# Optimization experiments

Measured on AMD Instinct MI355X. Metric: run time of the kernel, lower is better.

Reference implementation:

```python
import jax, jax.numpy as jnp
import numpy as np

# dims
B, T, C = 8, 2048, 768          # batch, tokens, n_embed
E, K, H = 8, 2, 3072            # n_experts, top_k, n_mlp_hidden
LOAD = 1.25
CAP = int(LOAD * K * T // E)    # expert_capacity = 640
N_LAYER = 12


def setup_inputs() -> dict:
    key = jax.random.key(0)
    ks = jax.random.split(key, 6)
    s = 0.02
    s_proj = 0.02 * (2 * N_LAYER) ** (-0.5)
    return {
        "x": jax.random.normal(ks[0], (B, T, C), jnp.float32),
        "w_router": (jax.random.normal(ks[1], (C, E), jnp.float32) * s),
        "b_router": jnp.zeros((E,), jnp.float32),
        "w_c_fc": (jax.random.normal(ks[2], (E, C, H), jnp.float32) * s),
        "b_c_fc": jnp.zeros((E, 1, H), jnp.float32),
        "w_gate": (jax.random.normal(ks[3], (E, C, H), jnp.float32) * s),
        "b_gate": jnp.zeros((E, 1, H), jnp.float32),
        "w_c_proj": (jax.random.normal(ks[4], (E, H, C), jnp.float32) * s_proj),
        "b_c_proj": jnp.zeros((E, 1, C), jnp.float32),
    }


def _route(xb, probs):
    """Per-sequence top-k routing + capacity-based scatter dispatch.
    xb: [T, C], probs: [T, E] -> (topk_probs [T,K], pos [T,K], ei [T,K], buf [E,CAP,C])"""
    topk_probs, idx = jax.lax.top_k(probs, K)          # [T, K]
    ei = jnp.swapaxes(idx, 0, 1).ravel()               # [K*T], k-major like original
    oh = jax.nn.one_hot(ei, E, dtype=jnp.int32)        # [K*T, E]
    pos = jnp.cumsum(oh, axis=0) * oh - 1              # running slot per expert
    pos = jnp.max(jnp.swapaxes(pos.reshape(K, T, E), 0, 1), axis=2)  # [T, K]
    ei = jnp.swapaxes(ei.reshape(K, T), 0, 1)          # [T, K]
    xr = jnp.repeat(xb, K, axis=0)                     # [T*K, C], token-major
    # out-of-capacity positions (>= CAP) are dropped by jax scatter semantics,
    # matching the original module.
    buf = jnp.zeros((E, CAP, C), xb.dtype).at[ei.ravel(), pos.ravel()].set(xr)
    return topk_probs, pos, ei, buf


def reference(x, w_router, b_router, w_c_fc, b_c_fc, w_gate, b_gate,
              w_c_proj, b_c_proj):
    gate_logits = jnp.einsum("btc,ce->bte", x, w_router) + b_router
    gate_probs = jax.nn.softmax(gate_logits)
    topk_probs, pos, ei, buf = jax.vmap(_route)(x, gate_probs)  # buf: [B,E,CAP,C]

    # dispatch: expert-major layout (token permutation inside each expert is
    # irrelevant for the per-token expert MLP, so this is equivalent to the
    # original's sharding-oriented reshuffle)
    expert_inputs = jnp.swapaxes(buf, 0, 1).reshape(E, B * CAP, C)

    # grouped-GEMM SwiGLU experts
    h = jnp.einsum("eti,eih->eth", expert_inputs, w_c_fc) + b_c_fc
    g = jnp.einsum("eti,eih->eth", expert_inputs, w_gate) + b_gate
    o = jnp.einsum("eth,eho->eto", jax.nn.silu(h * g), w_c_proj) + b_c_proj

    eo = jnp.swapaxes(o.reshape(E, B, CAP, C), 0, 1)    # [B, E, CAP, C]

    def combine(eo_b, ei_b, pos_b, p_b):
        gathered = eo_b[ei_b, pos_b]                    # [T, K, C]
        return jnp.sum(p_b[..., None] * gathered, axis=1)

    return jax.vmap(combine)(eo, ei, pos, topk_probs)   # [B, T, C]
```

## Files before the change

### kernel.cpp

```cpp
#include <hip/hip_runtime.h>

typedef unsigned short u16;
typedef unsigned int u32;
using u16x4 = __attribute__((ext_vector_type(4))) u16;
using u16x8 = __attribute__((ext_vector_type(8))) u16;
using bf16x8 = __attribute__((ext_vector_type(8))) __bf16;
using f32x4 = __attribute__((ext_vector_type(4))) float;

#define B_ 8
#define T_ 2048
#define C_ 768
#define E_ 8
#define K_ 2
#define H_ 3072
#define CAP_ 640
#define M_ (B_ * CAP_)
#define HC_ 1024
#define NCHUNK_ (H_ / HC_)
#define OVF_MAX_ 32768

__device__ __forceinline__ u16 f2bf(float x) {
  u32 u = __float_as_uint(x);
  u32 r = (u + 0x7FFFu + ((u >> 16) & 1u)) >> 16;
  return (u16)r;
}
__device__ __forceinline__ float bf2f(u16 v) { return __uint_as_float(((u32)v) << 16); }

__device__ __forceinline__ void gl_lds16(const u16* g, u16* l) {
  __builtin_amdgcn_global_load_lds((const __attribute__((address_space(1))) u32*)g,
                                   (__attribute__((address_space(3))) u32*)l, 16, 0, 0);
}
__device__ __forceinline__ bf16x8 ldfrag(const u16* p) {
  return __builtin_bit_cast(bf16x8, *(const u16x8*)p);
}

__global__ void wconv_transpose(const float* __restrict__ in, u16* __restrict__ out,
                                int R, int Cc) {
  __shared__ float tile[32][33];
  const float* inE = in + (size_t)blockIdx.z * R * Cc;
  u16* outE = out + (size_t)blockIdx.z * R * Cc;
  int tx = threadIdx.x & 31, ty = threadIdx.x >> 5;
  int r0 = blockIdx.y * 32, c0 = blockIdx.x * 32;
#pragma unroll
  for (int j = 0; j < 4; j++)
    tile[ty + j * 8][tx] = inE[(size_t)(r0 + ty + j * 8) * Cc + (c0 + tx)];
  __syncthreads();
#pragma unroll
  for (int j = 0; j < 4; j++)
    outE[(size_t)(c0 + ty + j * 8) * R + (r0 + tx)] = f2bf(tile[tx][ty + j * 8]);
}

__global__ void router_kernel(const float* __restrict__ x, const float* __restrict__ wr,
                              const float* __restrict__ br, float* __restrict__ tkp,
                              int* __restrict__ tki) {
  int bt = (blockIdx.x << 2) | (threadIdx.x >> 6);
  int lane = threadIdx.x & 63;
  const float* xr = x + (size_t)bt * C_;
  double acc[E_];
#pragma unroll
  for (int e = 0; e < E_; e++) acc[e] = 0.0;
#pragma unroll
  for (int i = 0; i < C_ / 64; i++) {
    int c = lane + i * 64;
    float xv = xr[c];
    const float* w = wr + c * E_;
#pragma unroll
    for (int e = 0; e < E_; e++) acc[e] += (double)xv * (double)w[e];
  }
#pragma unroll
  for (int off = 32; off > 0; off >>= 1) {
#pragma unroll
    for (int e = 0; e < E_; e++) acc[e] += __shfl_xor(acc[e], off);
  }
  if (lane == 0) {
    double lg[E_];
#pragma unroll
    for (int e = 0; e < E_; e++) lg[e] = acc[e] + (double)br[e];
    int i0 = 0;
#pragma unroll
    for (int e = 1; e < E_; e++) if (lg[e] > lg[i0]) i0 = e;
    int i1 = (i0 == 0) ? 1 : 0;
#pragma unroll
    for (int e = 0; e < E_; e++) if (e != i0 && lg[e] > lg[i1]) i1 = e;
    double mx = lg[i0], s = 0.0, pv[E_];
#pragma unroll
    for (int e = 0; e < E_; e++) { pv[e] = exp(lg[e] - mx); s += pv[e]; }
    tkp[bt * 2 + 0] = (float)(pv[i0] / s);
    tkp[bt * 2 + 1] = (float)(pv[i1] / s);
    tki[bt * 2 + 0] = i0;
    tki[bt * 2 + 1] = i1;
  }
}

__global__ void pos_kernel(const int* __restrict__ tki, int* __restrict__ pos) {
  __shared__ int sc[256][9];
  int b = blockIdx.x;
  int tid = threadIdx.x;
  const int* tib = tki + (size_t)b * T_ * 2;
  int* pb = pos + (size_t)b * T_ * 2;
  int ids[16];
  int cnt[E_];
#pragma unroll
  for (int e = 0; e < E_; e++) cnt[e] = 0;
#pragma unroll
  for (int j = 0; j < 16; j++) {
    int i = tid * 16 + j;
    int k = i >> 11, t = i & (T_ - 1);
    int id = tib[t * 2 + k];
    ids[j] = id;
#pragma unroll
    for (int e = 0; e < E_; e++) cnt[e] += (id == e);
  }
#pragma unroll
  for (int e = 0; e < E_; e++) sc[tid][e] = cnt[e];
  __syncthreads();
  for (int off = 1; off < 256; off <<= 1) {
    int v[E_];
    if (tid >= off) {
#pragma unroll
      for (int e = 0; e < E_; e++) v[e] = sc[tid - off][e];
    }
    __syncthreads();
    if (tid >= off) {
#pragma unroll
      for (int e = 0; e < E_; e++) sc[tid][e] += v[e];
    }
    __syncthreads();
  }
  int base[E_];
#pragma unroll
  for (int e = 0; e < E_; e++) base[e] = (tid > 0) ? sc[tid - 1][e] : 0;
#pragma unroll
  for (int j = 0; j < 16; j++) {
    int i = tid * 16 + j;
    int k = i >> 11, t = i & (T_ - 1);
    int id = ids[j];
    int p = 0;
#pragma unroll
    for (int e = 0; e < E_; e++) p += (id == e) ? base[e] : 0;
    pb[t * 2 + k] = p;
#pragma unroll
    for (int e = 0; e < E_; e++) base[e] += (id == e);
  }
}

__global__ void clear_kernel(int* __restrict__ invt, int* __restrict__ ovfCnt) {
  int i = blockIdx.x * 256 + threadIdx.x;
  invt[i] = -1;
  if (i == 0) *ovfCnt = 0;
}

__global__ void dispatch_kernel(const float* __restrict__ x, const int* __restrict__ tki,
                                const int* __restrict__ pos, u16* __restrict__ Xd,
                                int* __restrict__ invt, int* __restrict__ ovfCnt,
                                int2* __restrict__ ovf) {
  int gw = (blockIdx.x << 2) | (threadIdx.x >> 6);
  int lane = threadIdx.x & 63;
  int bt = gw >> 1;
  int b = bt >> 11;
  int e = tki[gw];
  int p = pos[gw];
  if (p >= CAP_) {
    if (lane == 0) {
      int idx = atomicAdd(ovfCnt, 1);
      if (idx < OVF_MAX_) ovf[idx] = make_int2(bt, gw & 1);
    }
    return;
  }
  size_t row = (size_t)e * M_ + (size_t)b * CAP_ + p;
  if (lane == 0) invt[row] = gw;
  const f32x4* src = (const f32x4*)(x + (size_t)bt * C_);
  u16* dst = Xd + row * C_;
#pragma unroll
  for (int i = 0; i < 3; i++) {
    f32x4 v = src[lane + i * 64];
    u16x4 o;
    o.x = f2bf(v.x); o.y = f2bf(v.y); o.z = f2bf(v.z); o.w = f2bf(v.w);
    *(u16x4*)(dst + (size_t)(lane + i * 64) * 4) = o;
  }
}

__global__ void init_out_kernel(const float* __restrict__ tkp, const int* __restrict__ tki,
                                const float* __restrict__ bp, float* __restrict__ out) {
  int bt = (blockIdx.x << 2) | (threadIdx.x >> 6);
  int lane = threadIdx.x & 63;
  int e0 = tki[bt * 2], e1 = tki[bt * 2 + 1];
  float w0 = tkp[bt * 2], w1 = tkp[bt * 2 + 1];
  const f32x4* b0 = (const f32x4*)(bp + (size_t)e0 * C_);
  const f32x4* b1 = (const f32x4*)(bp + (size_t)e1 * C_);
  f32x4* orow = (f32x4*)(out + (size_t)bt * C_);
#pragma unroll
  for (int i = 0; i < 3; i++) {
    int c = lane + i * 64;
    orow[c] = w0 * b0[c] + w1 * b1[c];
  }
}

__global__ __launch_bounds__(256, 2) void gemm_fc_gate(
    const u16* __restrict__ Xd, const u16* __restrict__ WfcT, const u16* __restrict__ WgT,
    const float* __restrict__ bfc, const float* __restrict__ bg, u16* __restrict__ S,
    int hc) {
  __shared__ __align__(16) u16 lds[2][3][128 * 32];
  const int NWG = E_ * 40 * (HC_ / 128);
  int bid0 = blockIdx.x;
  int bid = (bid0 & 7) * (NWG >> 3) + (bid0 >> 3);
  int e = bid / (40 * (HC_ / 128));
  int t = bid % (40 * (HC_ / 128));
  int tm = t / (HC_ / 128), tn = t % (HC_ / 128);
  int tid = threadIdx.x;
  int lane = tid & 63, wv = tid >> 6;
  int wm = wv & 1, wn = wv >> 1;
  int lr = lane & 15, quad = lane >> 4;

  const u16* XdE = Xd + (size_t)e * M_ * C_;
  const u16* B1E = WfcT + ((size_t)e * H_ + (size_t)hc * HC_) * C_;
  const u16* B2E = WgT + ((size_t)e * H_ + (size_t)hc * HC_) * C_;

  int rhalf = tid >> 2;
  int chunk = tid & 3;
  int swzc = chunk ^ ((rhalf >> 1) & 3);
  const u16* gA0 = XdE + (size_t)(tm * 128 + rhalf) * C_ + swzc * 8;
  const u16* gA1 = gA0 + 64 * C_;
  const u16* gB10 = B1E + (size_t)(tn * 128 + rhalf) * C_ + swzc * 8;
  const u16* gB11 = gB10 + 64 * C_;
  const u16* gB20 = B2E + (size_t)(tn * 128 + rhalf) * C_ + swzc * 8;
  const u16* gB21 = gB20 + 64 * C_;
  int ldsW0 = (wv * 16) * 32;
  int ldsW1 = (64 + wv * 16) * 32;

  f32x4 acc1[4][4], acc2[4][4];
#pragma unroll
  for (int i = 0; i < 4; i++)
#pragma unroll
    for (int j = 0; j < 4; j++) {
      acc1[i][j] = (f32x4){0.f, 0.f, 0.f, 0.f};
      acc2[i][j] = (f32x4){0.f, 0.f, 0.f, 0.f};
    }

  const int NK = C_ / 32;
  int rs = (quad ^ ((lr >> 1) & 3)) * 8;

  {
    gl_lds16(gA0, &lds[0][0][0] + ldsW0);
    gl_lds16(gA1, &lds[0][0][0] + ldsW1);
    gl_lds16(gB10, &lds[0][1][0] + ldsW0);
    gl_lds16(gB11, &lds[0][1][0] + ldsW1);
    gl_lds16(gB20, &lds[0][2][0] + ldsW0);
    gl_lds16(gB21, &lds[0][2][0] + ldsW1);
  }
  __syncthreads();

  int cur = 0;
  for (int kt = 0; kt < NK; kt++) {
    if (kt + 1 < NK) {
      int ko = (kt + 1) * 32;
      int nb = cur ^ 1;
      gl_lds16(gA0 + ko, &lds[nb][0][0] + ldsW0);
      gl_lds16(gA1 + ko, &lds[nb][0][0] + ldsW1);
      gl_lds16(gB10 + ko, &lds[nb][1][0] + ldsW0);
      gl_lds16(gB11 + ko, &lds[nb][1][0] + ldsW1);
      gl_lds16(gB20 + ko, &lds[nb][2][0] + ldsW0);
      gl_lds16(gB21 + ko, &lds[nb][2][0] + ldsW1);
    }
    bf16x8 af[4], b1f[4], b2f[4];
#pragma unroll
    for (int i = 0; i < 4; i++) {
      af[i] = ldfrag(&lds[cur][0][0] + (wm * 64 + i * 16 + lr) * 32 + rs);
      b1f[i] = ldfrag(&lds[cur][1][0] + (wn * 64 + i * 16 + lr) * 32 + rs);
      b2f[i] = ldfrag(&lds[cur][2][0] + (wn * 64 + i * 16 + lr) * 32 + rs);
    }
#pragma unroll
    for (int i = 0; i < 4; i++)
#pragma unroll
      for (int j = 0; j < 4; j++) {
        acc1[i][j] = __builtin_amdgcn_mfma_f32_16x16x32_bf16(af[i], b1f[j], acc1[i][j], 0, 0, 0);
        acc2[i][j] = __builtin_amdgcn_mfma_f32_16x16x32_bf16(af[i], b2f[j], acc2[i][j], 0, 0, 0);
      }
    __syncthreads();
    cur ^= 1;
  }

  u16* Se = S + (size_t)e * M_ * HC_;
  const float* bfcE = bfc + (size_t)e * H_ + (size_t)hc * HC_;
  const float* bgE = bg + (size_t)e * H_ + (size_t)hc * HC_;
  int col0 = tn * 128 + wn * 64 + lr;
  int row0 = tm * 128 + wm * 64 + quad * 4;
#pragma unroll
  for (int j = 0; j < 4; j++) {
    int col = col0 + j * 16;
    float bf_ = bfcE[col], bg_ = bgE[col];
#pragma unroll
    for (int i = 0; i < 4; i++) {
      int row = row0 + i * 16;
#pragma unroll
      for (int r = 0; r < 4; r++) {
        float h = acc1[i][j][r] + bf_;
        float g = acc2[i][j][r] + bg_;
        float z = h * g;
        float sv = z / (1.f + __expf(-z));
        Se[(size_t)(row + r) * HC_ + col] = f2bf(sv);
      }
    }
  }
}

__global__ __launch_bounds__(256, 3) void gemm_proj_scatter(
    const u16* __restrict__ S, const u16* __restrict__ WpT,
    const int* __restrict__ invt, const float* __restrict__ tkp,
    const int* __restrict__ tki, const int* __restrict__ ovfCnt,
    const int2* __restrict__ ovf, float* __restrict__ out, int hc) {
  __shared__ __align__(16) u16 lds[2][2][128 * 32];
  const int NWG = E_ * 40 * 6;
  int bid0 = blockIdx.x;
  int bid = (bid0 & 7) * (NWG >> 3) + (bid0 >> 3);
  int e = bid / (40 * 6);
  int t = bid % (40 * 6);
  int tm = t / 6, tn = t % 6;
  int tid = threadIdx.x;
  int lane = tid & 63, wv = tid >> 6;
  int wm = wv & 1, wn = wv >> 1;
  int lr = lane & 15, quad = lane >> 4;

  const u16* SE = S + (size_t)e * M_ * HC_;
  const u16* BE = WpT + (size_t)e * C_ * H_ + (size_t)hc * HC_;

  int rhalf = tid >> 2;
  int chunk = tid & 3;
  int swzc = chunk ^ ((rhalf >> 1) & 3);
  const u16* gA0 = SE + (size_t)(tm * 128 + rhalf) * HC_ + swzc * 8;
  const u16* gA1 = gA0 + 64 * HC_;
  const u16* gB0 = BE + (size_t)(tn * 128 + rhalf) * H_ + swzc * 8;
  const u16* gB1 = gB0 + 64 * H_;
  int ldsW0 = (wv * 16) * 32;
  int ldsW1 = (64 + wv * 16) * 32;

  f32x4 acc[4][4];
#pragma unroll
  for (int i = 0; i < 4; i++)
#pragma unroll
    for (int j = 0; j < 4; j++) acc[i][j] = (f32x4){0.f, 0.f, 0.f, 0.f};

  const int NK = HC_ / 32;
  int rs = (quad ^ ((lr >> 1) & 3)) * 8;

  {
    gl_lds16(gA0, &lds[0][0][0] + ldsW0);
    gl_lds16(gA1, &lds[0][0][0] + ldsW1);
    gl_lds16(gB0, &lds[0][1][0] + ldsW0);
    gl_lds16(gB1, &lds[0][1][0] + ldsW1);
  }
  __syncthreads();

  int cur = 0;
  for (int kt = 0; kt < NK; kt++) {
    if (kt + 1 < NK) {
      int ko = (kt + 1) * 32;
      int nb = cur ^ 1;
      gl_lds16(gA0 + ko, &lds[nb][0][0] + ldsW0);
      gl_lds16(gA1 + ko, &lds[nb][0][0] + ldsW1);
      gl_lds16(gB0 + ko, &lds[nb][1][0] + ldsW0);
      gl_lds16(gB1 + ko, &lds[nb][1][0] + ldsW1);
    }
    bf16x8 af[4], bf[4];
#pragma unroll
    for (int i = 0; i < 4; i++) {
      af[i] = ldfrag(&lds[cur][0][0] + (wm * 64 + i * 16 + lr) * 32 + rs);
      bf[i] = ldfrag(&lds[cur][1][0] + (wn * 64 + i * 16 + lr) * 32 + rs);
    }
#pragma unroll
    for (int i = 0; i < 4; i++)
#pragma unroll
      for (int j = 0; j < 4; j++)
        acc[i][j] = __builtin_amdgcn_mfma_f32_16x16x32_bf16(af[i], bf[j], acc[i][j], 0, 0, 0);
    __syncthreads();
    cur ^= 1;
  }

  int col0 = tn * 128 + wn * 64 + lr;
  int row0 = tm * 128 + wm * 64 + quad * 4;
  const int* invtE = invt + e * M_;
#pragma unroll
  for (int i = 0; i < 4; i++) {
#pragma unroll
    for (int r = 0; r < 4; r++) {
      int re = row0 + i * 16 + r;
      int g = invtE[re];
      if (g >= 0) {
        float w = tkp[g];
        float* orow = out + (size_t)(g >> 1) * C_;
#pragma unroll
        for (int j = 0; j < 4; j++)
          atomicAdd(orow + col0 + j * 16, w * acc[i][j][r]);
      }
    }
  }
  if (wm == 1 && quad == 3 && (tm % 5) == 4) {
    int b = tm / 5;
    int nov = *ovfCnt;
    if (nov > OVF_MAX_) nov = OVF_MAX_;
    for (int o = 0; o < nov; o++) {
      int2 en = ovf[o];
      int gw2 = en.x * 2 + en.y;
      if (tki[gw2] == e && (en.x >> 11) == b) {
        float w = tkp[gw2];
        float* orow = out + (size_t)en.x * C_;
#pragma unroll
        for (int j = 0; j < 4; j++)
          atomicAdd(orow + col0 + j * 16, w * acc[3][j][3]);
      }
    }
  }
}

extern "C" void kernel_launch(void* const* d_in, const int* in_sizes, int n_in,
                              void* d_out, int out_size, void* d_ws, size_t ws_size,
                              hipStream_t stream) {
  (void)in_sizes; (void)n_in; (void)out_size; (void)ws_size;
  const float* x = (const float*)d_in[0];
  const float* w_router = (const float*)d_in[1];
  const float* b_router = (const float*)d_in[2];
  const float* w_c_fc = (const float*)d_in[3];
  const float* b_c_fc = (const float*)d_in[4];
  const float* w_gate = (const float*)d_in[5];
  const float* b_gate = (const float*)d_in[6];
  const float* w_c_proj = (const float*)d_in[7];
  const float* b_c_proj = (const float*)d_in[8];
  float* out = (float*)d_out;

  char* p = (char*)d_ws;
  auto alloc = [&](size_t n) { char* r = p; p += (n + 255) & ~(size_t)255; return r; };
  const size_t WN = (size_t)E_ * C_ * H_;
  u16* WfcT = (u16*)alloc(WN * 2);
  u16* WgT = (u16*)alloc(WN * 2);
  u16* WpT = (u16*)alloc(WN * 2);
  u16* Xd = (u16*)alloc((size_t)E_ * M_ * C_ * 2);
  float* tkp = (float*)alloc((size_t)B_ * T_ * 2 * 4);
  int* tki = (int*)alloc((size_t)B_ * T_ * 2 * 4);
  int* pos = (int*)alloc((size_t)B_ * T_ * 2 * 4);
  int* invt = (int*)alloc((size_t)E_ * M_ * 4);
  int* ovfCnt = (int*)alloc(4);
  int2* ovf = (int2*)alloc((size_t)OVF_MAX_ * 8);
  u16* S = (u16*)alloc((size_t)E_ * M_ * HC_ * 2);

  dim3 blk(256);
  wconv_transpose<<<dim3(H_ / 32, C_ / 32, E_), blk, 0, stream>>>(w_c_fc, WfcT, C_, H_);
  wconv_transpose<<<dim3(H_ / 32, C_ / 32, E_), blk, 0, stream>>>(w_gate, WgT, C_, H_);
  wconv_transpose<<<dim3(C_ / 32, H_ / 32, E_), blk, 0, stream>>>(w_c_proj, WpT, H_, C_);

  router_kernel<<<dim3(B_ * T_ / 4), blk, 0, stream>>>(x, w_router, b_router, tkp, tki);
  pos_kernel<<<dim3(B_), blk, 0, stream>>>(tki, pos);
  clear_kernel<<<dim3(E_ * M_ / 256), blk, 0, stream>>>(invt, ovfCnt);
  dispatch_kernel<<<dim3(B_ * T_ * K_ / 4), blk, 0, stream>>>(x, tki, pos, Xd, invt, ovfCnt, ovf);
  init_out_kernel<<<dim3(B_ * T_ / 4), blk, 0, stream>>>(tkp, tki, b_c_proj, out);

  for (int hc = 0; hc < NCHUNK_; hc++) {
    gemm_fc_gate<<<dim3(E_ * 40 * (HC_ / 128)), blk, 0, stream>>>(
        Xd, WfcT, WgT, b_c_fc, b_gate, S, hc);
    gemm_proj_scatter<<<dim3(E_ * 40 * 6), blk, 0, stream>>>(
        S, WpT, invt, tkp, tki, ovfCnt, ovf, out, hc);
  }
}
```

Measured before the change: 1.150 ms.

## Triple-buffer LDS in both expert GEMMs with explicit vmcnt waits and setprio

Both the fc/gate GEMM and the projection GEMM go from double-buffered to triple-buffered LDS staging. Loads are issued two k-steps ahead, and partial s_waitcnt vmcnt waits replace the full __syncthreads, so one barrier per iteration now guards both read-after-write and buffer reuse. MFMA sections are wrapped in s_setprio to favour math waves. This aims to hide more global-load latency, at the cost of more LDS per block (72KB for fc_gate, 48KB for proj), which may limit occupancy under the launch bounds of 2 and 3.

```diff
diff --git a/kernel.cpp b/kernel.cpp
--- a/kernel.cpp
+++ b/kernel.cpp
@@ -200,7 +200,7 @@
     const u16* __restrict__ Xd, const u16* __restrict__ WfcT, const u16* __restrict__ WgT,
     const float* __restrict__ bfc, const float* __restrict__ bg, u16* __restrict__ S,
     int hc) {
-  __shared__ __align__(16) u16 lds[2][3][128 * 32];
+  __shared__ __align__(16) u16 lds[3][3][128 * 32];
   const int NWG = E_ * 40 * (HC_ / 128);
   int bid0 = blockIdx.x;
   int bid = (bid0 & 7) * (NWG >> 3) + (bid0 >> 3);
@@ -228,6 +228,16 @@
   int ldsW0 = (wv * 16) * 32;
   int ldsW1 = (64 + wv * 16) * 32;
 
+  auto stage = [&](int kt, int b) {
+    int ko = kt * 32;
+    gl_lds16(gA0 + ko, &lds[b][0][0] + ldsW0);
+    gl_lds16(gA1 + ko, &lds[b][0][0] + ldsW1);
+    gl_lds16(gB10 + ko, &lds[b][1][0] + ldsW0);
+    gl_lds16(gB11 + ko, &lds[b][1][0] + ldsW1);
+    gl_lds16(gB20 + ko, &lds[b][2][0] + ldsW0);
+    gl_lds16(gB21 + ko, &lds[b][2][0] + ldsW1);
+  };
+
   f32x4 acc1[4][4], acc2[4][4];
 #pragma unroll
   for (int i = 0; i < 4; i++)
@@ -240,27 +250,18 @@
   const int NK = C_ / 32;
   int rs = (quad ^ ((lr >> 1) & 3)) * 8;
 
-  {
-    gl_lds16(gA0, &lds[0][0][0] + ldsW0);
-    gl_lds16(gA1, &lds[0][0][0] + ldsW1);
-    gl_lds16(gB10, &lds[0][1][0] + ldsW0);
-    gl_lds16(gB11, &lds[0][1][0] + ldsW1);
-    gl_lds16(gB20, &lds[0][2][0] + ldsW0);
-    gl_lds16(gB21, &lds[0][2][0] + ldsW1);
-  }
-  __syncthreads();
+  stage(0, 0);
+  stage(1, 1);
 
   int cur = 0;
   for (int kt = 0; kt < NK; kt++) {
-    if (kt + 1 < NK) {
-      int ko = (kt + 1) * 32;
-      int nb = cur ^ 1;
-      gl_lds16(gA0 + ko, &lds[nb][0][0] + ldsW0);
-      gl_lds16(gA1 + ko, &lds[nb][0][0] + ldsW1);
-      gl_lds16(gB10 + ko, &lds[nb][1][0] + ldsW0);
-      gl_lds16(gB11 + ko, &lds[nb][1][0] + ldsW1);
-      gl_lds16(gB20 + ko, &lds[nb][2][0] + ldsW0);
-      gl_lds16(gB21 + ko, &lds[nb][2][0] + ldsW1);
+    if (kt < NK - 1) asm volatile("s_waitcnt vmcnt(6)" ::: "memory");
+    else             asm volatile("s_waitcnt vmcnt(0)" ::: "memory");
+    __builtin_amdgcn_s_barrier();
+    __builtin_amdgcn_sched_barrier(0);
+    if (kt + 2 < NK) {
+      int nb = cur + 2; if (nb >= 3) nb -= 3;
+      stage(kt + 2, nb);
     }
     bf16x8 af[4], b1f[4], b2f[4];
 #pragma unroll
@@ -269,6 +270,7 @@
       b1f[i] = ldfrag(&lds[cur][1][0] + (wn * 64 + i * 16 + lr) * 32 + rs);
       b2f[i] = ldfrag(&lds[cur][2][0] + (wn * 64 + i * 16 + lr) * 32 + rs);
     }
+    __builtin_amdgcn_s_setprio(1);
 #pragma unroll
     for (int i = 0; i < 4; i++)
 #pragma unroll
@@ -276,8 +278,8 @@
         acc1[i][j] = __builtin_amdgcn_mfma_f32_16x16x32_bf16(af[i], b1f[j], acc1[i][j], 0, 0, 0);
         acc2[i][j] = __builtin_amdgcn_mfma_f32_16x16x32_bf16(af[i], b2f[j], acc2[i][j], 0, 0, 0);
       }
-    __syncthreads();
-    cur ^= 1;
+    __builtin_amdgcn_s_setprio(0);
+    cur = cur + 1; if (cur >= 3) cur -= 3;
   }
 
   u16* Se = S + (size_t)e * M_ * HC_;
@@ -309,7 +311,7 @@
     const int* __restrict__ invt, const float* __restrict__ tkp,
     const int* __restrict__ tki, const int* __restrict__ ovfCnt,
     const int2* __restrict__ ovf, float* __restrict__ out, int hc) {
-  __shared__ __align__(16) u16 lds[2][2][128 * 32];
+  __shared__ __align__(16) u16 lds[3][2][128 * 32];
   const int NWG = E_ * 40 * 6;
   int bid0 = blockIdx.x;
   int bid = (bid0 & 7) * (NWG >> 3) + (bid0 >> 3);
@@ -334,6 +336,14 @@
   int ldsW0 = (wv * 16) * 32;
   int ldsW1 = (64 + wv * 16) * 32;
 
+  auto stage = [&](int kt, int b) {
+    int ko = kt * 32;
+    gl_lds16(gA0 + ko, &lds[b][0][0] + ldsW0);
+    gl_lds16(gA1 + ko, &lds[b][0][0] + ldsW1);
+    gl_lds16(gB0 + ko, &lds[b][1][0] + ldsW0);
+    gl_lds16(gB1 + ko, &lds[b][1][0] + ldsW1);
+  };
+
   f32x4 acc[4][4];
 #pragma unroll
   for (int i = 0; i < 4; i++)
@@ -343,23 +353,18 @@
   const int NK = HC_ / 32;
   int rs = (quad ^ ((lr >> 1) & 3)) * 8;
 
-  {
-    gl_lds16(gA0, &lds[0][0][0] + ldsW0);
-    gl_lds16(gA1, &lds[0][0][0] + ldsW1);
-    gl_lds16(gB0, &lds[0][1][0] + ldsW0);
-    gl_lds16(gB1, &lds[0][1][0] + ldsW1);
-  }
-  __syncthreads();
+  stage(0, 0);
+  stage(1, 1);
 
   int cur = 0;
   for (int kt = 0; kt < NK; kt++) {
-    if (kt + 1 < NK) {
-      int ko = (kt + 1) * 32;
-      int nb = cur ^ 1;
-      gl_lds16(gA0 + ko, &lds[nb][0][0] + ldsW0);
-      gl_lds16(gA1 + ko, &lds[nb][0][0] + ldsW1);
-      gl_lds16(gB0 + ko, &lds[nb][1][0] + ldsW0);
-      gl_lds16(gB1 + ko, &lds[nb][1][0] + ldsW1);
+    if (kt < NK - 1) asm volatile("s_waitcnt vmcnt(4)" ::: "memory");
+    else             asm volatile("s_waitcnt vmcnt(0)" ::: "memory");
+    __builtin_amdgcn_s_barrier();
+    __builtin_amdgcn_sched_barrier(0);
+    if (kt + 2 < NK) {
+      int nb = cur + 2; if (nb >= 3) nb -= 3;
+      stage(kt + 2, nb);
     }
     bf16x8 af[4], bf[4];
 #pragma unroll
@@ -367,13 +372,14 @@
       af[i] = ldfrag(&lds[cur][0][0] + (wm * 64 + i * 16 + lr) * 32 + rs);
       bf[i] = ldfrag(&lds[cur][1][0] + (wn * 64 + i * 16 + lr) * 32 + rs);
     }
+    __builtin_amdgcn_s_setprio(1);
 #pragma unroll
     for (int i = 0; i < 4; i++)
 #pragma unroll
       for (int j = 0; j < 4; j++)
         acc[i][j] = __builtin_amdgcn_mfma_f32_16x16x32_bf16(af[i], bf[j], acc[i][j], 0, 0, 0);
-    __syncthreads();
-    cur ^= 1;
+    __builtin_amdgcn_s_setprio(0);
+    cur = cur + 1; if (cur >= 3) cur -= 3;
   }
 
   int col0 = tn * 128 + wn * 64 + lr;
```

Result: faster. 1.105 ms (-4.0%).
